# Kernel tuning notes

Hardware: AMD Instinct MI355X
Metric: run time of the kernel (lower is better)

Reference implementation:

```python
import jax, jax.numpy as jnp
import numpy as np

D_MODEL = 512
D_HEAD = 64
N_HEADS = D_MODEL // D_HEAD  # 8
KSIZE = 7


def setup_inputs() -> dict:
    key = jax.random.key(0)
    k1, k2, k3 = jax.random.split(key, 3)
    x = jax.random.normal(k1, (2, 48, 48, D_MODEL), dtype=jnp.float32)
    # torch Linear(d, 3d, bias=False): y = x @ W.T ; store transposed weight directly
    w_qkv = jax.random.normal(k2, (D_MODEL, 3 * D_MODEL), dtype=jnp.float32) * 0.02
    w_out = jax.random.normal(k3, (D_MODEL, D_MODEL), dtype=jnp.float32) * 0.02
    return {"x": x, "w_qkv": w_qkv, "w_out": w_out}


def _nbhd_idx(L, k):
    # NATTEN semantics: window centered at each pixel, shifted (clamped) to stay
    # fully inside the image near borders. Returns [L, k] absolute indices.
    start = jnp.clip(jnp.arange(L) - k // 2, 0, L - k)
    return start[:, None] + jnp.arange(k)[None, :]


def reference(x, w_qkv, w_out):
    n, h, w, _ = x.shape
    qkv = (x @ w_qkv).reshape(n, h, w, 3, N_HEADS, D_HEAD)
    qkv = jnp.transpose(qkv, (3, 0, 4, 1, 2, 5))  # [3, n, nh, h, w, e]
    q, k, v = qkv[0], qkv[1], qkv[2]
    q = q / jnp.asarray(D_HEAD, q.dtype) ** 0.5

    ih = _nbhd_idx(h, KSIZE)  # [h, k]
    iw = _nbhd_idx(w, KSIZE)  # [w, k]
    IH = ih[:, None, :, None]  # [h,1,k,1]
    IW = iw[None, :, None, :]  # [1,w,1,k]

    # gather per-pixel 2D neighborhoods: [n, nh, h, w, ka, kb, e]
    k_nb = k[:, :, IH, IW, :]
    logits = jnp.einsum('nghwe,nghwabe->nghwab', q, k_nb)
    logits = logits.reshape(n, N_HEADS, h, w, KSIZE * KSIZE)
    attn = jax.nn.softmax(logits, axis=-1).reshape(n, N_HEADS, h, w, KSIZE, KSIZE)

    v_nb = v[:, :, IH, IW, :]
    o = jnp.einsum('nghwab,nghwabe->nghwe', attn, v_nb)  # [n, nh, h, w, e]
    o = jnp.transpose(o, (0, 2, 3, 1, 4)).reshape(n, h, w, N_HEADS * D_HEAD)
    return o @ w_out
```

## Files before the change

kernel.cpp:

```cpp
#include <hip/hip_runtime.h>
#include <hip/hip_bf16.h>

typedef __bf16 bf16x4 __attribute__((ext_vector_type(4)));
typedef __bf16 bf16x8 __attribute__((ext_vector_type(8)));
typedef float f32x4 __attribute__((ext_vector_type(4)));

#define N_PIX 4608
#define D_MODEL 512
#define QKV_N 1536

__device__ __forceinline__ void gload_lds16(const void* g, void* l) {
  __builtin_amdgcn_global_load_lds(
      (const __attribute__((address_space(1))) unsigned int*)g,
      (__attribute__((address_space(3))) unsigned int*)l, 16, 0, 0);
}

__global__ __launch_bounds__(256) void prep_kernel(
    const float* __restrict__ x, const float* __restrict__ wq,
    const float* __restrict__ wo, __bf16* __restrict__ xbf,
    __bf16* __restrict__ wqT, __bf16* __restrict__ woT) {
  int b = blockIdx.x, tid = threadIdx.x;
  if (b < 2304) {
    int i = b * 1024 + tid * 4;
    float4 v = *(const float4*)&x[i];
    bf16x4 o = {(__bf16)v.x, (__bf16)v.y, (__bf16)v.z, (__bf16)v.w};
    *(bf16x4*)&xbf[i] = o;
    return;
  }
  __shared__ float tile[32][33];
  const float* src; __bf16* dst; int R, C, bx, by;
  bool is_wq;
  if (b < 3072) {
    int t = b - 2304; src = wq; dst = wqT; R = 512; C = 1536;
    bx = (t % 48) * 32; by = (t / 48) * 32; is_wq = true;
  } else {
    int t = b - 3072; src = wo; dst = woT; R = 512; C = 512;
    bx = (t & 15) * 32; by = (t >> 4) * 32; is_wq = false;
  }
  int tx = tid & 31, ty = tid >> 5;
#pragma unroll
  for (int i = 0; i < 32; i += 8)
    tile[ty + i][tx] = src[(by + ty + i) * C + bx + tx];
  __syncthreads();
#pragma unroll
  for (int i = 0; i < 32; i += 8) {
    int outrow = bx + ty + i;
    float v = tile[tx][ty + i];
    if (is_wq && outrow < 512) v *= 0.125f;
    dst[outrow * R + by + tx] = (__bf16)v;
  }
}

template <int BM, int BN>
__global__ __launch_bounds__(256) void gemm_kernel(
    const __bf16* __restrict__ A, const __bf16* __restrict__ Bt,
    void* __restrict__ C, int M, int N, int K, int c_is_f32) {
  constexpr int MT = BM / 32;
  constexpr int NT = BN / 32;
  constexpr int AR = BM / 4;
  constexpr int BR = BN / 4;
  __shared__ __bf16 sA[2][BM * 32];
  __shared__ __bf16 sB[2][BN * 32];
  int tid = threadIdx.x;
  int wv = tid >> 6, lane = tid & 63;
  int quad = lane >> 4, r16 = lane & 15;
  int m0 = blockIdx.y * BM, n0 = blockIdx.x * BN;

  int rA = lane >> 2;
  int kc = (lane & 3) * 8;
  const __bf16* Ag0 = A + (long)(m0 + wv * AR + rA) * K + kc;
  const __bf16* Bg0 = Bt + (long)(n0 + wv * BR + rA) * K + kc;

  int mw = (wv & 1) * (BM / 2), nw = (wv >> 1) * (BN / 2);

  f32x4 acc[MT][NT];
#pragma unroll
  for (int mt = 0; mt < MT; ++mt)
#pragma unroll
    for (int nt = 0; nt < NT; ++nt) acc[mt][nt] = f32x4{0.f, 0.f, 0.f, 0.f};

  auto stage = [&](int buf, int k0) {
    gload_lds16(Ag0 + k0, &sA[buf][(wv * AR) * 32]);
    if (AR == 32)
      gload_lds16(Ag0 + (long)16 * K + k0, &sA[buf][(wv * AR + 16) * 32]);
    gload_lds16(Bg0 + k0, &sB[buf][(wv * BR) * 32]);
    if (BR == 32)
      gload_lds16(Bg0 + (long)16 * K + k0, &sB[buf][(wv * BR + 16) * 32]);
  };

  stage(0, 0);
  int cur = 0;
  for (int k0 = 0; k0 < K; k0 += 32) {
    __syncthreads();
    if (k0 + 32 < K) stage(cur ^ 1, k0 + 32);
    bf16x8 af[MT], bfr[NT];
#pragma unroll
    for (int mt = 0; mt < MT; ++mt)
      af[mt] = *(const bf16x8*)&sA[cur][(mw + mt * 16 + r16) * 32 + quad * 8];
#pragma unroll
    for (int nt = 0; nt < NT; ++nt)
      bfr[nt] = *(const bf16x8*)&sB[cur][(nw + nt * 16 + r16) * 32 + quad * 8];
#pragma unroll
    for (int mt = 0; mt < MT; ++mt)
#pragma unroll
      for (int nt = 0; nt < NT; ++nt)
        acc[mt][nt] = __builtin_amdgcn_mfma_f32_16x16x32_bf16(af[mt], bfr[nt], acc[mt][nt], 0, 0, 0);
    cur ^= 1;
  }

  __bf16* Cb = (__bf16*)C;
  float* Cf = (float*)C;
#pragma unroll
  for (int mt = 0; mt < MT; ++mt)
#pragma unroll
    for (int r = 0; r < 4; ++r) {
      int row = m0 + mw + mt * 16 + quad * 4 + r;
#pragma unroll
      for (int nt = 0; nt < NT; ++nt) {
        int col = n0 + nw + nt * 16 + r16;
        float v = acc[mt][nt][r];
        if (c_is_f32) Cf[(long)row * N + col] = v;
        else          Cb[(long)row * N + col] = (__bf16)v;
      }
    }
}

__global__ __launch_bounds__(256) void natten_attn_kernel(
    const __bf16* __restrict__ qkv, __bf16* __restrict__ o) {
  __shared__ __bf16 sKP[16384];
  __shared__ __bf16 sVT[16384];
  __shared__ __bf16 sQ[4096];
  char* kB = (char*)sKP;
  char* vB = (char*)sVT;
  char* qB = (char*)sQ;

  int tid = threadIdx.x;
  int lane = tid & 63, wv = tid >> 6;
  int quad = lane >> 4, r16 = lane & 15;
  int bid = blockIdx.x;
  int nB = bid / 288;
  int rem = bid - nB * 288;
  int head = rem / 36;
  int tile = rem - head * 36;
  int tr = tile / 6, tc = tile - tr * 6;
  int r0 = tr * 8, c0 = tc * 8;
  int loH = r0 - 3; loH = loH < 0 ? 0 : (loH > 41 ? 41 : loH);
  int loW = c0 - 3; loW = loW < 0 ? 0 : (loW > 41 ? 41 : loW);
  long hb = (long)head * 64;

  {
    int rl = lane >> 3, cc = lane & 7;
#pragma unroll
    for (int it = 0; it < 7; ++it) {
      int g = wv * 7 + it;
      int row = g * 8 + rl;
      int pos = row > 195 ? 195 : row;
      int pr = pos / 14, pc = pos - pr * 14;
      int hh = loH + pr; hh = hh > 47 ? 47 : hh;
      int wp = loW + pc; wp = wp > 47 ? 47 : wp;
      int csrc = cc ^ (row & 7);
      const __bf16* src = qkv + (long)(nB * 2304 + hh * 48 + wp) * QKV_N + 512 + hb + csrc * 8;
      gload_lds16(src, kB + g * 1024);
    }
#pragma unroll
    for (int it = 0; it < 2; ++it) {
      int g = wv * 2 + it;
      int row = g * 8 + rl;
      int csrc = cc ^ (row & 7);
      int pix = nB * 2304 + (r0 + (row >> 3)) * 48 + c0 + (row & 7);
      const __bf16* src = qkv + (long)pix * QKV_N + hb + csrc * 8;
      gload_lds16(src, qB + g * 1024);
    }
  }
#pragma unroll
  for (int it = 0; it < 7; ++it) {
    int idx = tid + it * 256;
    int pos = idx >> 3, cb = idx & 7;
    int pp = pos > 195 ? 195 : pos;
    int pr = pp / 14, pc = pp - pr * 14;
    int hh = loH + pr; hh = hh > 47 ? 47 : hh;
    int wp = loW + pc; wp = wp > 47 ? 47 : wp;
    bf16x8 v = *(const bf16x8*)(qkv + (long)(nB * 2304 + hh * 48 + wp) * QKV_N + 1024 + hb + cb * 8);
#pragma unroll
    for (int i = 0; i < 8; ++i) {
      int ch = cb * 8 + i;
      *(__bf16*)(vB + ch * 512 + ((2 * pos) ^ ((ch & 7) << 4))) = v[i];
    }
  }
  __syncthreads();

  int rowq = wv * 16 + r16;
  int swq = (rowq & 7) << 4;
  bf16x8 aq0 = *(const bf16x8*)(qB + rowq * 128 + ((quad * 16) ^ swq));
  bf16x8 aq1 = *(const bf16x8*)(qB + rowq * 128 + ((64 + quad * 16) ^ swq));
  f32x4 acc[14];
#pragma unroll
  for (int nt = 0; nt < 14; ++nt) acc[nt] = f32x4{0.f, 0.f, 0.f, 0.f};
#pragma unroll
  for (int nt = 0; nt < 14; ++nt) {
    int rk = nt * 16 + r16;
    int swk = (rk & 7) << 4;
    bf16x8 b0 = *(const bf16x8*)(kB + rk * 128 + ((quad * 16) ^ swk));
    bf16x8 b1 = *(const bf16x8*)(kB + rk * 128 + ((64 + quad * 16) ^ swk));
    acc[nt] = __builtin_amdgcn_mfma_f32_16x16x32_bf16(aq0, b0, acc[nt], 0, 0, 0);
    acc[nt] = __builtin_amdgcn_mfma_f32_16x16x32_bf16(aq1, b1, acc[nt], 0, 0, 0);
  }

  int hs[4], wsX[4];
#pragma unroll
  for (int r = 0; r < 4; ++r) {
    int q = wv * 16 + quad * 4 + r;
    int h = r0 + (q >> 3), w = c0 + (q & 7);
    int a = h - 3; a = a < 0 ? 0 : (a > 41 ? 41 : a);
    int b = w - 3; b = b < 0 ? 0 : (b > 41 ? 41 : b);
    hs[r] = a - loH; wsX[r] = b - loW;
  }
  {
    int pr = r16 >= 14 ? 1 : 0;
    int pc = r16 - pr * 14;
#pragma unroll
    for (int nt = 0; nt < 14; ++nt) {
      bool pv = (nt * 16 + r16) < 196;
#pragma unroll
      for (int r = 0; r < 4; ++r) {
        bool ok = pv && (unsigned)(pr - hs[r]) <= 6u && (unsigned)(pc - wsX[r]) <= 6u;
        acc[nt][r] = ok ? acc[nt][r] : -1e30f;
      }
      pc += 2; pr += 1;
      if (pc >= 14) { pc -= 14; pr += 1; }
    }
  }
  float inv[4];
#pragma unroll
  for (int r = 0; r < 4; ++r) {
    float m = acc[0][r];
#pragma unroll
    for (int nt = 1; nt < 14; ++nt) m = fmaxf(m, acc[nt][r]);
    m = fmaxf(m, __shfl_xor(m, 1));
    m = fmaxf(m, __shfl_xor(m, 2));
    m = fmaxf(m, __shfl_xor(m, 4));
    m = fmaxf(m, __shfl_xor(m, 8));
    float s = 0.f;
#pragma unroll
    for (int nt = 0; nt < 14; ++nt) { float e = __expf(acc[nt][r] - m); acc[nt][r] = e; s += e; }
    s += __shfl_xor(s, 1);
    s += __shfl_xor(s, 2);
    s += __shfl_xor(s, 4);
    s += __shfl_xor(s, 8);
    inv[r] = 1.f / s;
  }
  __syncthreads();

#pragma unroll
  for (int r = 0; r < 4; ++r) {
    int q = wv * 16 + quad * 4 + r;
    char* rowp = kB + q * 512;
    int sw = (q & 7) << 4;
#pragma unroll
    for (int nt = 0; nt < 14; ++nt) {
      int pos = nt * 16 + r16;
      *(__bf16*)(rowp + ((2 * pos) ^ sw)) = (__bf16)acc[nt][r];
    }
  }
  __syncthreads();

  f32x4 acc2[4];
#pragma unroll
  for (int nt = 0; nt < 4; ++nt) acc2[nt] = f32x4{0.f, 0.f, 0.f, 0.f};
#pragma unroll
  for (int ks = 0; ks < 7; ++ks) {
    bf16x8 ap = *(const bf16x8*)(kB + rowq * 512 + ((ks * 64 + quad * 16) ^ swq));
#pragma unroll
    for (int nt = 0; nt < 4; ++nt) {
      int rc = nt * 16 + r16;
      bf16x8 bv = *(const bf16x8*)(vB + rc * 512 + ((ks * 64 + quad * 16) ^ ((rc & 7) << 4)));
      acc2[nt] = __builtin_amdgcn_mfma_f32_16x16x32_bf16(ap, bv, acc2[nt], 0, 0, 0);
    }
  }

#pragma unroll
  for (int r = 0; r < 4; ++r) {
    int q = wv * 16 + quad * 4 + r;
    long pix = nB * 2304 + (long)(r0 + (q >> 3)) * 48 + c0 + (q & 7);
    __bf16* op = o + pix * D_MODEL + hb;
    float iv = inv[r];
#pragma unroll
    for (int nt = 0; nt < 4; ++nt)
      op[nt * 16 + r16] = (__bf16)(acc2[nt][r] * iv);
  }
}


extern "C" void kernel_launch(void* const* d_in, const int* in_sizes, int n_in,
                              void* d_out, int out_size, void* d_ws, size_t ws_size,
                              hipStream_t stream) {
  const float* x = (const float*)d_in[0];
  const float* w_qkv = (const float*)d_in[1];
  const float* w_out = (const float*)d_in[2];
  float* out = (float*)d_out;

  __bf16* ws = (__bf16*)d_ws;
  __bf16* xbf   = ws;
  __bf16* wqkvT = xbf + N_PIX * D_MODEL;
  __bf16* woutT = wqkvT + QKV_N * D_MODEL;
  __bf16* qkvb  = woutT + D_MODEL * D_MODEL;
  __bf16* obf   = qkvb + N_PIX * QKV_N;

  prep_kernel<<<3328, 256, 0, stream>>>(x, w_qkv, w_out, xbf, wqkvT, woutT);
  gemm_kernel<128, 128><<<dim3(QKV_N / 128, N_PIX / 128), 256, 0, stream>>>(
      xbf, wqkvT, qkvb, N_PIX, QKV_N, D_MODEL, 0);
  natten_attn_kernel<<<576, 256, 0, stream>>>(qkvb, obf);
  gemm_kernel<64, 128><<<dim3(D_MODEL / 128, N_PIX / 64), 256, 0, stream>>>(
      obf, woutT, out, N_PIX, D_MODEL, D_MODEL, 1);
}
```

Baseline: 115.2 us.

## Double GEMM K-tile to 64 with XOR-swizzled LDS and smaller block tiles

The GEMM now stages a K-slice of 64 instead of 32 per iteration, which halves the number of barriers and loop iterations. The LDS layout uses an XOR swizzle on 16-byte chunks so the fragment reads avoid bank conflicts. The QKV GEMM tile shrinks from 128x128 to 64x128 and the output GEMM from 64x128 to 64x64, launching more blocks to fill the CUs. The costs are more LDS per block and less operand reuse per block.

Measured after the change: 112.0 us. 1.03x faster.

```diff
diff --git a/kernel.cpp b/kernel.cpp
--- a/kernel.cpp
+++ b/kernel.cpp
@@ -55,21 +55,20 @@
 __global__ __launch_bounds__(256) void gemm_kernel(
     const __bf16* __restrict__ A, const __bf16* __restrict__ Bt,
     void* __restrict__ C, int M, int N, int K, int c_is_f32) {
+  constexpr int BK = 64;
   constexpr int MT = BM / 32;
   constexpr int NT = BN / 32;
-  constexpr int AR = BM / 4;
-  constexpr int BR = BN / 4;
-  __shared__ __bf16 sA[2][BM * 32];
-  __shared__ __bf16 sB[2][BN * 32];
+  constexpr int NGA = BM / 8;
+  constexpr int NGB = BN / 8;
+  constexpr int NG = (NGA + NGB) / 4;
+  __shared__ __bf16 sA[2][BM * BK];
+  __shared__ __bf16 sB[2][BN * BK];
   int tid = threadIdx.x;
   int wv = tid >> 6, lane = tid & 63;
   int quad = lane >> 4, r16 = lane & 15;
   int m0 = blockIdx.y * BM, n0 = blockIdx.x * BN;
-
-  int rA = lane >> 2;
-  int kc = (lane & 3) * 8;
-  const __bf16* Ag0 = A + (long)(m0 + wv * AR + rA) * K + kc;
-  const __bf16* Bg0 = Bt + (long)(n0 + wv * BR + rA) * K + kc;
+  int rl = lane >> 3, cc = lane & 7;
+  int csrc = (cc ^ rl) * 8;
 
   int mw = (wv & 1) * (BM / 2), nw = (wv >> 1) * (BN / 2);
 
@@ -80,31 +79,53 @@
     for (int nt = 0; nt < NT; ++nt) acc[mt][nt] = f32x4{0.f, 0.f, 0.f, 0.f};
 
   auto stage = [&](int buf, int k0) {
-    gload_lds16(Ag0 + k0, &sA[buf][(wv * AR) * 32]);
-    if (AR == 32)
-      gload_lds16(Ag0 + (long)16 * K + k0, &sA[buf][(wv * AR + 16) * 32]);
-    gload_lds16(Bg0 + k0, &sB[buf][(wv * BR) * 32]);
-    if (BR == 32)
-      gload_lds16(Bg0 + (long)16 * K + k0, &sB[buf][(wv * BR + 16) * 32]);
+#pragma unroll
+    for (int i = 0; i < NG; ++i) {
+      int g = wv + i * 4;
+      if (g < NGA) {
+        int row = g * 8 + rl;
+        gload_lds16(A + (long)(m0 + row) * K + k0 + csrc,
+                    (char*)sA[buf] + g * 1024);
+      } else {
+        int g2 = g - NGA;
+        int row = g2 * 8 + rl;
+        gload_lds16(Bt + (long)(n0 + row) * K + k0 + csrc,
+                    (char*)sB[buf] + g2 * 1024);
+      }
+    }
   };
 
   stage(0, 0);
   int cur = 0;
-  for (int k0 = 0; k0 < K; k0 += 32) {
+  for (int k0 = 0; k0 < K; k0 += BK) {
     __syncthreads();
-    if (k0 + 32 < K) stage(cur ^ 1, k0 + 32);
-    bf16x8 af[MT], bfr[NT];
-#pragma unroll
-    for (int mt = 0; mt < MT; ++mt)
-      af[mt] = *(const bf16x8*)&sA[cur][(mw + mt * 16 + r16) * 32 + quad * 8];
-#pragma unroll
-    for (int nt = 0; nt < NT; ++nt)
-      bfr[nt] = *(const bf16x8*)&sB[cur][(nw + nt * 16 + r16) * 32 + quad * 8];
-#pragma unroll
-    for (int mt = 0; mt < MT; ++mt)
-#pragma unroll
-      for (int nt = 0; nt < NT; ++nt)
-        acc[mt][nt] = __builtin_amdgcn_mfma_f32_16x16x32_bf16(af[mt], bfr[nt], acc[mt][nt], 0, 0, 0);
+    if (k0 + BK < K) stage(cur ^ 1, k0 + BK);
+    const char* aB = (const char*)sA[cur];
+    const char* bB = (const char*)sB[cur];
+    bf16x8 af[2][MT], bfr[2][NT];
+#pragma unroll
+    for (int ks = 0; ks < 2; ++ks) {
+#pragma unroll
+      for (int mt = 0; mt < MT; ++mt) {
+        int row = mw + mt * 16 + r16;
+        af[ks][mt] = *(const bf16x8*)(aB + row * 128 +
+                       ((ks * 64 + quad * 16) ^ ((row & 7) << 4)));
+      }
+#pragma unroll
+      for (int nt = 0; nt < NT; ++nt) {
+        int row = nw + nt * 16 + r16;
+        bfr[ks][nt] = *(const bf16x8*)(bB + row * 128 +
+                        ((ks * 64 + quad * 16) ^ ((row & 7) << 4)));
+      }
+    }
+#pragma unroll
+    for (int ks = 0; ks < 2; ++ks)
+#pragma unroll
+      for (int mt = 0; mt < MT; ++mt)
+#pragma unroll
+        for (int nt = 0; nt < NT; ++nt)
+          acc[mt][nt] = __builtin_amdgcn_mfma_f32_16x16x32_bf16(
+              af[ks][mt], bfr[ks][nt], acc[mt][nt], 0, 0, 0);
     cur ^= 1;
   }
 
@@ -307,9 +328,9 @@
   __bf16* obf   = qkvb + N_PIX * QKV_N;
 
   prep_kernel<<<3328, 256, 0, stream>>>(x, w_qkv, w_out, xbf, wqkvT, woutT);
-  gemm_kernel<128, 128><<<dim3(QKV_N / 128, N_PIX / 128), 256, 0, stream>>>(
+  gemm_kernel<64, 128><<<dim3(QKV_N / 128, N_PIX / 64), 256, 0, stream>>>(
       xbf, wqkvT, qkvb, N_PIX, QKV_N, D_MODEL, 0);
   natten_attn_kernel<<<576, 256, 0, stream>>>(qkvb, obf);
-  gemm_kernel<64, 128><<<dim3(D_MODEL / 128, N_PIX / 64), 256, 0, stream>>>(
+  gemm_kernel<64, 64><<<dim3(D_MODEL / 64, N_PIX / 64), 256, 0, stream>>>(
       obf, woutT, out, N_PIX, D_MODEL, D_MODEL, 1);
 }
```
